# Optimization experiments

Measured on AMD Instinct MI355X. Metric: run time of the kernel, lower is better.

Reference implementation:

```python
import jax, jax.numpy as jnp
import numpy as np

DIM = 1024
N_HEADS = 16
HEAD_DIM = DIM // N_HEADS
FREQS = [31.0, 37.0, 41.0, 43.0, 47.0]
TWO_PI = 2.0 * float(np.pi)


def setup_inputs() -> dict:
    key = jax.random.key(0)
    ks = jax.random.split(key, 16)
    B, L = 2, 1024
    s = 0.02
    inp = {
        'x': jax.random.normal(ks[0], (B, L, DIM), dtype=jnp.float32),
        'Wq': jax.random.normal(ks[1], (DIM, DIM), dtype=jnp.float32) * s,
        'bq': jnp.zeros((DIM,), dtype=jnp.float32),
        'Wk': jax.random.normal(ks[2], (DIM, DIM), dtype=jnp.float32) * s,
        'bk': jnp.zeros((DIM,), dtype=jnp.float32),
        'Wv': jax.random.normal(ks[3], (DIM, DIM), dtype=jnp.float32) * s,
        'bv': jnp.zeros((DIM,), dtype=jnp.float32),
        'Wo': jax.random.normal(ks[4], (DIM, DIM), dtype=jnp.float32) * s,
        'bo': jnp.zeros((DIM,), dtype=jnp.float32),
        'alpha': jax.random.normal(ks[5], (N_HEADS, len(FREQS)), dtype=jnp.float32) * 0.1,
        'phi': jax.random.uniform(ks[6], (N_HEADS, len(FREQS)), dtype=jnp.float32) * TWO_PI,
        'temperature': jnp.ones((1,), dtype=jnp.float32),
        'gamma': jnp.ones((DIM,), dtype=jnp.float32),
        'beta': jnp.zeros((DIM,), dtype=jnp.float32),
    }
    return inp


def reference(x, Wq, bq, Wk, bk, Wv, bv, Wo, bo, alpha, phi, temperature, gamma, beta):
    B, L, D = x.shape
    H, hd = N_HEADS, HEAD_DIM
    # projections (torch Linear: y = x @ W.T + b), split heads -> (B,H,L,hd)
    q = (x @ Wq.T + bq).reshape(B, L, H, hd).transpose(0, 2, 1, 3)
    k = (x @ Wk.T + bk).reshape(B, L, H, hd).transpose(0, 2, 1, 3)
    v = (x @ Wv.T + bv).reshape(B, L, H, hd).transpose(0, 2, 1, 3)
    # similarity (B,H,L,L)
    sim = jnp.einsum('bhid,bhjd->bhij', q, k) / jnp.sqrt(jnp.asarray(hd, x.dtype))
    temp = jnp.abs(temperature)[0] + 0.1
    sim = sim / temp
    # multi-frequency holographic scores: sum_f alpha_f * sin(2*pi*sim/p_f + phi_f)
    scores = jnp.zeros_like(sim)
    for fi, freq in enumerate(FREQS):
        a = alpha[:, fi][None, :, None, None]
        p = phi[:, fi][None, :, None, None]
        scores = scores + a * jnp.sin(TWO_PI * sim / freq + p)
    # sigmoid-sum normalization (not softmax)
    w = jax.nn.sigmoid(scores)
    w = w / (jnp.sum(w, axis=-1, keepdims=True) + 1e-10)
    out = jnp.einsum('bhij,bhjd->bhid', w, v)
    out = out.transpose(0, 2, 1, 3).reshape(B, L, D)
    out = out @ Wo.T + bo
    # LayerNorm (eps=1e-5, biased variance)
    mu = jnp.mean(out, axis=-1, keepdims=True)
    var = jnp.mean(jnp.square(out - mu), axis=-1, keepdims=True)
    return (out - mu) / jnp.sqrt(var + 1e-5) * gamma + beta
```

## Files before the change

kernel.cpp:

```cpp
#include <hip/hip_runtime.h>
#include <hip/hip_bf16.h>

typedef short bf16x8 __attribute__((ext_vector_type(8)));
typedef float f32x4 __attribute__((ext_vector_type(4)));

#define MFMA16(a, b, c) __builtin_amdgcn_mfma_f32_16x16x32_bf16(a, b, c, 0, 0, 0)

static constexpr int SEQ = 1024;
static constexpr int DIM = 1024;
static constexpr int NH = 16;
static constexpr int HD = 64;

#if __has_builtin(__builtin_amdgcn_rcpf)
#define FAST_RCP(x) __builtin_amdgcn_rcpf(x)
#else
#define FAST_RCP(x) (1.0f / (x))
#endif

#if __has_builtin(__builtin_amdgcn_exp2f)
#define EXP2F(x) __builtin_amdgcn_exp2f(x)
#else
#define EXP2F(x) exp2f(x)
#endif

__device__ __forceinline__ int swz(int r) { return r ^ (r >> 3); }

__device__ __forceinline__ void gload16(const __hip_bfloat16* g, __hip_bfloat16* l)
{
    typedef const __attribute__((address_space(1))) unsigned GU;
    typedef __attribute__((address_space(3))) unsigned LU;
    __builtin_amdgcn_global_load_lds((GU*)g, (LU*)l, 16, 0, 0);
}

__global__ __launch_bounds__(256) void cvt_all(
    const float* __restrict__ x,  const float* __restrict__ wq,
    const float* __restrict__ wk, const float* __restrict__ wv,
    const float* __restrict__ wo,
    __hip_bfloat16* __restrict__ xb,  __hip_bfloat16* __restrict__ wqb,
    __hip_bfloat16* __restrict__ wkb, __hip_bfloat16* __restrict__ wvb,
    __hip_bfloat16* __restrict__ wob)
{
    const int reg = blockIdx.y;
    const float* src; __hip_bfloat16* dst; int n;
    if      (reg == 0) { src = x;  dst = xb;  n = 2 * SEQ * DIM; }
    else if (reg == 1) { src = wq; dst = wqb; n = DIM * DIM; }
    else if (reg == 2) { src = wk; dst = wkb; n = DIM * DIM; }
    else if (reg == 3) { src = wv; dst = wvb; n = DIM * DIM; }
    else               { src = wo; dst = wob; n = DIM * DIM; }
    const int i = (blockIdx.x * 256 + threadIdx.x) * 4;
    if (i < n) {
        float4 v = *(const float4*)(src + i);
        __hip_bfloat16 t[4];
        t[0] = __float2bfloat16(v.x); t[1] = __float2bfloat16(v.y);
        t[2] = __float2bfloat16(v.z); t[3] = __float2bfloat16(v.w);
        *(ushort4*)(dst + i) = *(ushort4*)t;
    }
}

__global__ __launch_bounds__(256) void gemm_qkv(
    const __hip_bfloat16* __restrict__ A,
    const __hip_bfloat16* __restrict__ W0, const __hip_bfloat16* __restrict__ W1,
    const __hip_bfloat16* __restrict__ W2,
    const float* __restrict__ b0, const float* __restrict__ b1,
    const float* __restrict__ b2,
    __hip_bfloat16* __restrict__ Y0, __hip_bfloat16* __restrict__ Y1,
    __hip_bfloat16* __restrict__ Y2,
    int M, int N, int K)
{
    __shared__ __align__(16) __hip_bfloat16 As[64 * 32];
    __shared__ __align__(16) __hip_bfloat16 Ws[128 * 32];

    const int z = blockIdx.z;
    const __hip_bfloat16* W = (z == 0) ? W0 : ((z == 1) ? W1 : W2);
    const float* bias = (z == 0) ? b0 : ((z == 1) ? b1 : b2);
    __hip_bfloat16* Y = (z == 0) ? Y0 : ((z == 1) ? Y1 : Y2);

    const int tid = threadIdx.x;
    const int wv = tid >> 6, lane = tid & 63;
    const int col16 = lane & 15, quad = lane >> 4;
    const int m0 = blockIdx.x * 64, n0 = blockIdx.y * 128;

    const __hip_bfloat16* ga = A + (size_t)(m0 + (tid >> 2)) * K + (tid & 3) * 8;
    const __hip_bfloat16* gb = W + (size_t)(n0 + (tid >> 2)) * K + (tid & 3) * 8;
    __hip_bfloat16* lA = As + wv * 512;
    __hip_bfloat16* lB = Ws + wv * 512;

    const int wr = wv >> 1, wc = wv & 1;
    const __hip_bfloat16* ar = As + (wr * 32 + col16) * 32 + quad * 8;
    const __hip_bfloat16* br = Ws + (wc * 64 + col16) * 32 + quad * 8;

    f32x4 acc[8] = {};

    for (int k0 = 0; k0 < K; k0 += 32) {
        gload16(ga + k0,                  lA);
        gload16(gb + k0,                  lB);
        gload16(gb + k0 + (size_t)64 * K, lB + 2048);
        __syncthreads();
        bf16x8 af[2], bfm[4];
#pragma unroll
        for (int mt = 0; mt < 2; ++mt) af[mt] = *(const bf16x8*)(ar + mt * 16 * 32);
#pragma unroll
        for (int nt = 0; nt < 4; ++nt) bfm[nt] = *(const bf16x8*)(br + nt * 16 * 32);
#pragma unroll
        for (int mt = 0; mt < 2; ++mt)
#pragma unroll
            for (int nt = 0; nt < 4; ++nt)
                acc[mt * 4 + nt] = MFMA16(af[mt], bfm[nt], acc[mt * 4 + nt]);
        __syncthreads();
    }

#pragma unroll
    for (int nt = 0; nt < 4; ++nt) {
        const int n = n0 + wc * 64 + nt * 16 + col16;
        const float bv = bias[n];
#pragma unroll
        for (int mt = 0; mt < 2; ++mt) {
#pragma unroll
            for (int r = 0; r < 4; ++r) {
                const int m = m0 + wr * 32 + mt * 16 + quad * 4 + r;
                Y[(size_t)m * N + n] = __float2bfloat16(acc[mt * 4 + nt][r] + bv);
            }
        }
    }
}

__global__ __launch_bounds__(256) void gemm_osplit(
    const __hip_bfloat16* __restrict__ A,
    const __hip_bfloat16* __restrict__ W,
    const float* __restrict__ bias,
    float* __restrict__ Y0, float* __restrict__ Y1,
    int M, int N, int K)
{
    __shared__ __align__(16) __hip_bfloat16 As[64 * 32];
    __shared__ __align__(16) __hip_bfloat16 Ws[128 * 32];

    const int z = blockIdx.z;
    float* Y = (z == 0) ? Y0 : Y1;
    const int kb = z * 512;

    const int tid = threadIdx.x;
    const int wv = tid >> 6, lane = tid & 63;
    const int col16 = lane & 15, quad = lane >> 4;
    const int m0 = blockIdx.x * 64, n0 = blockIdx.y * 128;

    const __hip_bfloat16* ga = A + (size_t)(m0 + (tid >> 2)) * K + (tid & 3) * 8 + kb;
    const __hip_bfloat16* gb = W + (size_t)(n0 + (tid >> 2)) * K + (tid & 3) * 8 + kb;
    __hip_bfloat16* lA = As + wv * 512;
    __hip_bfloat16* lB = Ws + wv * 512;

    const int wr = wv >> 1, wc = wv & 1;
    const __hip_bfloat16* ar = As + (wr * 32 + col16) * 32 + quad * 8;
    const __hip_bfloat16* br = Ws + (wc * 64 + col16) * 32 + quad * 8;

    f32x4 acc[8] = {};

    for (int k0 = 0; k0 < 512; k0 += 32) {
        gload16(ga + k0,                  lA);
        gload16(gb + k0,                  lB);
        gload16(gb + k0 + (size_t)64 * K, lB + 2048);
        __syncthreads();
        bf16x8 af[2], bfm[4];
#pragma unroll
        for (int mt = 0; mt < 2; ++mt) af[mt] = *(const bf16x8*)(ar + mt * 16 * 32);
#pragma unroll
        for (int nt = 0; nt < 4; ++nt) bfm[nt] = *(const bf16x8*)(br + nt * 16 * 32);
#pragma unroll
        for (int mt = 0; mt < 2; ++mt)
#pragma unroll
            for (int nt = 0; nt < 4; ++nt)
                acc[mt * 4 + nt] = MFMA16(af[mt], bfm[nt], acc[mt * 4 + nt]);
        __syncthreads();
    }

#pragma unroll
    for (int nt = 0; nt < 4; ++nt) {
        const int n = n0 + wc * 64 + nt * 16 + col16;
        const float bv = (z == 0) ? bias[n] : 0.0f;
#pragma unroll
        for (int mt = 0; mt < 2; ++mt) {
#pragma unroll
            for (int r = 0; r < 4; ++r) {
                const int m = m0 + wr * 32 + mt * 16 + quad * 4 + r;
                Y[(size_t)m * N + n] = acc[mt * 4 + nt][r] + bv;
            }
        }
    }
}

__global__ __launch_bounds__(256) void attn_kernel(
    const __hip_bfloat16* __restrict__ Q,
    const __hip_bfloat16* __restrict__ K,
    const __hip_bfloat16* __restrict__ V,
    const float* __restrict__ alpha, const float* __restrict__ phi,
    const float* __restrict__ temperature,
    __hip_bfloat16* __restrict__ AO)
{
    __shared__ __align__(16) char smem[18432 + 5120];
    __hip_bfloat16* VtBase = (__hip_bfloat16*)smem;
    __hip_bfloat16* PlBase = (__hip_bfloat16*)(smem + 18432);
    float* Ocomb = (float*)smem;
    float* Dl    = (float*)(smem + 2 * 16 * 68 * 4);

    const int tid = threadIdx.x;
    const int wv = tid >> 6, lane = tid & 63;
    const int col16 = lane & 15, quad = lane >> 4;
    const int g = wv & 1, half = wv >> 1;

    const int bh = blockIdx.y, b = bh >> 4, h = bh & 15;
    const int i0 = blockIdx.x * 32 + g * 16;
    const size_t base = ((size_t)b * SEQ) * DIM + (size_t)h * HD;

    const float tempv = fabsf(temperature[0]) + 0.1f;
    const float simscale = 1.0f / (8.0f * tempv);
    const float freqs[5] = {31.0f, 37.0f, 41.0f, 43.0f, 47.0f};

    float p[8] = {0.f, 0.f, 0.f, 0.f, 0.f, 0.f, 0.f, 0.f};
#pragma unroll
    for (int f = 0; f < 5; ++f) {
        const float a  = alpha[h * 5 + f] * 1.44269504089f;
        const float ph = phi[h * 5 + f];
        const float sp = __sinf(ph), cp = __cosf(ph);
        const float c  = 6.28318530718f * simscale / freqs[f];
        const float c2 = c * c, c3 = c2 * c, c4 = c2 * c2;
        const float c5 = c4 * c, c6 = c4 * c2, c7 = c4 * c3;
        p[0] += a * sp;
        p[1] += a * cp * c;
        p[2] -= a * sp * c2 * 0.5f;
        p[3] -= a * cp * c3 * (1.0f / 6.0f);
        p[4] += a * sp * c4 * (1.0f / 24.0f);
        p[5] += a * cp * c5 * (1.0f / 120.0f);
        p[6] -= a * sp * c6 * (1.0f / 720.0f);
        p[7] -= a * cp * c7 * (1.0f / 5040.0f);
    }

    const __hip_bfloat16* qrow = Q + base + (size_t)(i0 + col16) * DIM + quad * 8;
    const bf16x8 qa0 = *(const bf16x8*)(qrow);
    const bf16x8 qa1 = *(const bf16x8*)(qrow + 32);

    const __hip_bfloat16* kbase = K + base + (size_t)col16 * DIM + quad * 8;

    const int tl = tid & 127;
    const int sc0 = (tl & 7) * 8;
    const int sx  = tl & 7;
    const int jj0 = (tl >> 3) * 2;
    __hip_bfloat16* VtH = VtBase + half * 64 * 72;
    __hip_bfloat16* rowp[8];
#pragma unroll
    for (int e = 0; e < 8; ++e) rowp[e] = VtH + (sc0 + (e ^ sx)) * 72;

    const __hip_bfloat16* vrd[4];
#pragma unroll
    for (int t = 0; t < 4; ++t)
        vrd[t] = VtH + swz(t * 16 + col16) * 72 + quad * 8;

    __hip_bfloat16* PlW = PlBase + wv * 16 * 40;
    const __hip_bfloat16* plr = PlW + swz(col16) * 40 + quad * 8;
    __hip_bfloat16* plw[4];
#pragma unroll
    for (int r = 0; r < 4; ++r) plw[r] = PlW + swz(quad * 4 + r) * 40;

    f32x4 o[4] = {};
    float denom[4] = {0.f, 0.f, 0.f, 0.f};

    bf16x8 vr[2][2];
    bf16x8 kf[4][2];

    {
        const int j0 = half * 512;
#pragma unroll
        for (int s = 0; s < 2; ++s) {
            const __hip_bfloat16* vp = V + base + (size_t)(j0 + jj0 + 32 * s) * DIM + sc0;
            vr[s][0] = *(const bf16x8*)(vp);
            vr[s][1] = *(const bf16x8*)(vp + DIM);
        }
#pragma unroll
        for (int u = 0; u < 4; ++u) {
            const __hip_bfloat16* kp = kbase + (size_t)(j0 + u * 16) * DIM;
            kf[u][0] = *(const bf16x8*)(kp);
            kf[u][1] = *(const bf16x8*)(kp + 32);
        }
    }

    for (int it = 0; it < 8; ++it) {
        __syncthreads();
#pragma unroll
        for (int s = 0; s < 2; ++s) {
#pragma unroll
            for (int e = 0; e < 8; ++e) {
                unsigned pk = ((unsigned)(unsigned short)vr[s][0][e]) |
                              (((unsigned)(unsigned short)vr[s][1][e]) << 16);
                *(unsigned*)(rowp[e] + jj0 + 32 * s) = pk;
            }
        }
        __syncthreads();

        const int j1 = half * 512 + (it + 1) * 64;
        if (it < 7) {
#pragma unroll
            for (int s = 0; s < 2; ++s) {
                const __hip_bfloat16* vp = V + base + (size_t)(j1 + jj0 + 32 * s) * DIM + sc0;
                vr[s][0] = *(const bf16x8*)(vp);
                vr[s][1] = *(const bf16x8*)(vp + DIM);
            }
        }

        f32x4 sa4[4];
#pragma unroll
        for (int u = 0; u < 4; ++u) {
            f32x4 z = {};
            z = MFMA16(qa0, kf[u][0], z);
            z = MFMA16(qa1, kf[u][1], z);
            sa4[u] = z;
        }

        if (it < 7) {
#pragma unroll
            for (int u = 0; u < 4; ++u) {
                const __hip_bfloat16* kp = kbase + (size_t)(j1 + u * 16) * DIM;
                kf[u][0] = *(const bf16x8*)(kp);
                kf[u][1] = *(const bf16x8*)(kp + 32);
            }
        }

#pragma unroll
        for (int sub = 0; sub < 2; ++sub) {
#pragma unroll
            for (int s2 = 0; s2 < 2; ++s2) {
                const int u = sub * 2 + s2;
#pragma unroll
                for (int r = 0; r < 4; ++r) {
                    const float sv = sa4[u][r];
                    float sc = fmaf(sv, p[7], p[6]);
                    sc = fmaf(sv, sc, p[5]);
                    sc = fmaf(sv, sc, p[4]);
                    sc = fmaf(sv, sc, p[3]);
                    sc = fmaf(sv, sc, p[2]);
                    sc = fmaf(sv, sc, p[1]);
                    sc = fmaf(sv, sc, p[0]);
                    const float w = FAST_RCP(1.0f + EXP2F(-sc));
                    denom[r] += w;
                    plw[r][s2 * 16 + col16] = __float2bfloat16(w);
                }
            }
            bf16x8 pa = *(const bf16x8*)plr;
#pragma unroll
            for (int t = 0; t < 4; ++t) {
                bf16x8 vb = *(const bf16x8*)(vrd[t] + 32 * sub);
                o[t] = MFMA16(pa, vb, o[t]);
            }
        }
    }

#pragma unroll
    for (int r = 0; r < 4; ++r) {
        float d = denom[r];
        d += __shfl_xor(d, 1);
        d += __shfl_xor(d, 2);
        d += __shfl_xor(d, 4);
        d += __shfl_xor(d, 8);
        denom[r] = d;
    }

    __syncthreads();
    if (half == 1) {
#pragma unroll
        for (int t = 0; t < 4; ++t)
#pragma unroll
            for (int r = 0; r < 4; ++r)
                Ocomb[(g * 16 + quad * 4 + r) * 68 + t * 16 + col16] = o[t][r];
        if (col16 == 0) {
#pragma unroll
            for (int r = 0; r < 4; ++r) Dl[g * 16 + quad * 4 + r] = denom[r];
        }
    }
    __syncthreads();
    if (half == 0) {
#pragma unroll
        for (int r = 0; r < 4; ++r)
            denom[r] = denom[r] + Dl[g * 16 + quad * 4 + r] + 1e-10f;
#pragma unroll
        for (int t = 0; t < 4; ++t) {
#pragma unroll
            for (int r = 0; r < 4; ++r) {
                const float val =
                    (o[t][r] + Ocomb[(g * 16 + quad * 4 + r) * 68 + t * 16 + col16]) / denom[r];
                const size_t row = (size_t)b * SEQ + i0 + quad * 4 + r;
                AO[row * DIM + h * HD + t * 16 + col16] = __float2bfloat16(val);
            }
        }
    }
}

__global__ __launch_bounds__(256) void ln_kernel(
    const float* __restrict__ Yp0,
    const float* __restrict__ Yp1,
    const float* __restrict__ gamma,
    const float* __restrict__ beta,
    float* __restrict__ out)
{
    const int row = blockIdx.x;
    const float* y0 = Yp0 + (size_t)row * DIM;
    const float* y1 = Yp1 + (size_t)row * DIM;

    float v[4];
    float s = 0.f, s2 = 0.f;
#pragma unroll
    for (int e = 0; e < 4; ++e) {
        const int idx = threadIdx.x + e * 256;
        v[e] = y0[idx] + y1[idx];
        s += v[e];
        s2 += v[e] * v[e];
    }
#pragma unroll
    for (int off = 1; off < 64; off <<= 1) {
        s  += __shfl_xor(s, off);
        s2 += __shfl_xor(s2, off);
    }
    __shared__ float ps[4], ps2[4];
    const int wave = threadIdx.x >> 6;
    if ((threadIdx.x & 63) == 0) { ps[wave] = s; ps2[wave] = s2; }
    __syncthreads();
    s  = ps[0] + ps[1] + ps[2] + ps[3];
    s2 = ps2[0] + ps2[1] + ps2[2] + ps2[3];

    const float mu   = s * (1.0f / DIM);
    const float var  = s2 * (1.0f / DIM) - mu * mu;
    const float rstd = rsqrtf(var + 1e-5f);

#pragma unroll
    for (int e = 0; e < 4; ++e) {
        const int idx = threadIdx.x + e * 256;
        out[(size_t)row * DIM + idx] =
            (v[e] - mu) * rstd * gamma[idx] + beta[idx];
    }
}

extern "C" void kernel_launch(void* const* d_in, const int* in_sizes, int n_in,
                              void* d_out, int out_size, void* d_ws, size_t ws_size,
                              hipStream_t stream)
{
    const float* x     = (const float*)d_in[0];
    const float* Wq    = (const float*)d_in[1];
    const float* bq    = (const float*)d_in[2];
    const float* Wk    = (const float*)d_in[3];
    const float* bk    = (const float*)d_in[4];
    const float* Wv    = (const float*)d_in[5];
    const float* bv    = (const float*)d_in[6];
    const float* Wo    = (const float*)d_in[7];
    const float* bo    = (const float*)d_in[8];
    const float* alpha = (const float*)d_in[9];
    const float* phi   = (const float*)d_in[10];
    const float* temp  = (const float*)d_in[11];
    const float* gamma = (const float*)d_in[12];
    const float* beta  = (const float*)d_in[13];

    float* out = (float*)d_out;

    const int B = 2;
    const int M = B * SEQ;

    char* wsb = (char*)d_ws;
    __hip_bfloat16* xb  = (__hip_bfloat16*)(wsb + 0);
    __hip_bfloat16* Wqb = (__hip_bfloat16*)(wsb + (4u  << 20));
    __hip_bfloat16* Wkb = (__hip_bfloat16*)(wsb + (6u  << 20));
    __hip_bfloat16* Wvb = (__hip_bfloat16*)(wsb + (8u  << 20));
    __hip_bfloat16* Wob = (__hip_bfloat16*)(wsb + (10u << 20));
    __hip_bfloat16* Qb  = (__hip_bfloat16*)(wsb + (12u << 20));
    __hip_bfloat16* Kb  = (__hip_bfloat16*)(wsb + (16u << 20));
    __hip_bfloat16* Vb  = (__hip_bfloat16*)(wsb + (20u << 20));
    __hip_bfloat16* AO  = (__hip_bfloat16*)(wsb + (24u << 20));
    float*          Yp0 = (float*)(wsb + 0);
    float*          Yp1 = (float*)(wsb + (12u << 20));

    hipLaunchKernelGGL(cvt_all, dim3(2048, 5), dim3(256), 0, stream,
                       x, Wq, Wk, Wv, Wo, xb, Wqb, Wkb, Wvb, Wob);

    hipLaunchKernelGGL(gemm_qkv, dim3(M / 64, DIM / 128, 3), dim3(256), 0, stream,
                       xb, Wqb, Wkb, Wvb, bq, bk, bv, Qb, Kb, Vb, M, DIM, DIM);

    hipLaunchKernelGGL(attn_kernel, dim3(SEQ / 32, B * NH), dim3(256), 0, stream,
                       Qb, Kb, Vb, alpha, phi, temp, AO);

    hipLaunchKernelGGL(gemm_osplit, dim3(M / 64, DIM / 128, 2), dim3(256), 0, stream,
                       AO, Wob, bo, Yp0, Yp1, M, DIM, DIM);

    hipLaunchKernelGGL(ln_kernel, dim3(M), dim3(256), 0, stream,
                       Yp0, Yp1, gamma, beta, out);
}
```

Baseline: 177.7 us.

## Split attention key range across two blocks and add combine kernel

Adds a split-K style partition of the key dimension in the attention kernel via blockIdx.z, so each block covers half the keys and writes unnormalized fp32 partial outputs and denominators to workspace. A new combine kernel sums the partials, normalizes and writes bf16 AO. The intent is to double the number of attention blocks (from 1024 to 2048) for better occupancy and load balance on the CUs. The cost is an extra kernel launch and extra fp32 partial traffic, and the split path only runs when the workspace is at least 36 MB.

```diff
diff --git a/kernel.cpp b/kernel.cpp
--- a/kernel.cpp
+++ b/kernel.cpp
@@ -193,7 +193,9 @@
     const __hip_bfloat16* __restrict__ V,
     const float* __restrict__ alpha, const float* __restrict__ phi,
     const float* __restrict__ temperature,
-    __hip_bfloat16* __restrict__ AO)
+    float* __restrict__ Op0, float* __restrict__ Op1,
+    float* __restrict__ Dp0, float* __restrict__ Dp1,
+    __hip_bfloat16* __restrict__ AO, int nz)
 {
     __shared__ __align__(16) char smem[18432 + 5120];
     __hip_bfloat16* VtBase = (__hip_bfloat16*)smem;
@@ -209,6 +211,11 @@
     const int bh = blockIdx.y, b = bh >> 4, h = bh & 15;
     const int i0 = blockIdx.x * 32 + g * 16;
     const size_t base = ((size_t)b * SEQ) * DIM + (size_t)h * HD;
+
+    const int z = blockIdx.z;
+    const int jb = z * (SEQ / nz);
+    const int hrange = SEQ / nz / 2;
+    const int niter = hrange >> 6;
 
     const float tempv = fabsf(temperature[0]) + 0.1f;
     const float simscale = 1.0f / (8.0f * tempv);
@@ -266,7 +273,7 @@
     bf16x8 kf[4][2];
 
     {
-        const int j0 = half * 512;
+        const int j0 = jb + half * hrange;
 #pragma unroll
         for (int s = 0; s < 2; ++s) {
             const __hip_bfloat16* vp = V + base + (size_t)(j0 + jj0 + 32 * s) * DIM + sc0;
@@ -281,7 +288,7 @@
         }
     }
 
-    for (int it = 0; it < 8; ++it) {
+    for (int it = 0; it < niter; ++it) {
         __syncthreads();
 #pragma unroll
         for (int s = 0; s < 2; ++s) {
@@ -294,8 +301,8 @@
         }
         __syncthreads();
 
-        const int j1 = half * 512 + (it + 1) * 64;
-        if (it < 7) {
+        const int j1 = jb + half * hrange + (it + 1) * 64;
+        if (it + 1 < niter) {
 #pragma unroll
             for (int s = 0; s < 2; ++s) {
                 const __hip_bfloat16* vp = V + base + (size_t)(j1 + jj0 + 32 * s) * DIM + sc0;
@@ -307,13 +314,13 @@
         f32x4 sa4[4];
 #pragma unroll
         for (int u = 0; u < 4; ++u) {
-            f32x4 z = {};
-            z = MFMA16(qa0, kf[u][0], z);
-            z = MFMA16(qa1, kf[u][1], z);
-            sa4[u] = z;
-        }
-
-        if (it < 7) {
+            f32x4 zz = {};
+            zz = MFMA16(qa0, kf[u][0], zz);
+            zz = MFMA16(qa1, kf[u][1], zz);
+            sa4[u] = zz;
+        }
+
+        if (it + 1 < niter) {
 #pragma unroll
             for (int u = 0; u < 4; ++u) {
                 const __hip_bfloat16* kp = kbase + (size_t)(j1 + u * 16) * DIM;
@@ -375,20 +382,68 @@
     }
     __syncthreads();
     if (half == 0) {
-#pragma unroll
-        for (int r = 0; r < 4; ++r)
-            denom[r] = denom[r] + Dl[g * 16 + quad * 4 + r] + 1e-10f;
-#pragma unroll
-        for (int t = 0; t < 4; ++t) {
-#pragma unroll
-            for (int r = 0; r < 4; ++r) {
-                const float val =
-                    (o[t][r] + Ocomb[(g * 16 + quad * 4 + r) * 68 + t * 16 + col16]) / denom[r];
-                const size_t row = (size_t)b * SEQ + i0 + quad * 4 + r;
-                AO[row * DIM + h * HD + t * 16 + col16] = __float2bfloat16(val);
-            }
-        }
-    }
+        if (nz == 1) {
+#pragma unroll
+            for (int r = 0; r < 4; ++r)
+                denom[r] = denom[r] + Dl[g * 16 + quad * 4 + r] + 1e-10f;
+#pragma unroll
+            for (int t = 0; t < 4; ++t) {
+#pragma unroll
+                for (int r = 0; r < 4; ++r) {
+                    const float val =
+                        (o[t][r] + Ocomb[(g * 16 + quad * 4 + r) * 68 + t * 16 + col16]) / denom[r];
+                    const size_t row = (size_t)b * SEQ + i0 + quad * 4 + r;
+                    AO[row * DIM + h * HD + t * 16 + col16] = __float2bfloat16(val);
+                }
+            }
+        } else {
+            float* Op = (z == 0) ? Op0 : Op1;
+            float* Dp = (z == 0) ? Dp0 : Dp1;
+#pragma unroll
+            for (int r = 0; r < 4; ++r)
+                denom[r] = denom[r] + Dl[g * 16 + quad * 4 + r];
+            if (col16 == 0) {
+#pragma unroll
+                for (int r = 0; r < 4; ++r)
+                    Dp[(size_t)bh * SEQ + i0 + quad * 4 + r] = denom[r];
+            }
+#pragma unroll
+            for (int t = 0; t < 4; ++t) {
+#pragma unroll
+                for (int r = 0; r < 4; ++r) {
+                    const size_t prow = (size_t)bh * SEQ + i0 + quad * 4 + r;
+                    Op[prow * 64 + t * 16 + col16] =
+                        o[t][r] + Ocomb[(g * 16 + quad * 4 + r) * 68 + t * 16 + col16];
+                }
+            }
+        }
+    }
+}
+
+__global__ __launch_bounds__(256) void attn_combine(
+    const float* __restrict__ O0, const float* __restrict__ O1,
+    const float* __restrict__ D0, const float* __restrict__ D1,
+    __hip_bfloat16* __restrict__ AO)
+{
+    const int row = blockIdx.x;
+    const int b = row >> 10, i = row & 1023;
+    const int t = threadIdx.x;
+    const int h = t >> 4, dq = (t & 15) * 4;
+    const int bh = b * 16 + h;
+    const size_t prow = (size_t)bh * SEQ + i;
+    const size_t obase = prow * 64 + dq;
+
+    const float4 a0 = *(const float4*)(O0 + obase);
+    const float4 a1 = *(const float4*)(O1 + obase);
+    const float dn = D0[prow] + D1[prow] + 1e-10f;
+    const float rdn = 1.0f / dn;
+
+    __hip_bfloat16 tv[4];
+    tv[0] = __float2bfloat16((a0.x + a1.x) * rdn);
+    tv[1] = __float2bfloat16((a0.y + a1.y) * rdn);
+    tv[2] = __float2bfloat16((a0.z + a1.z) * rdn);
+    tv[3] = __float2bfloat16((a0.w + a1.w) * rdn);
+    *(ushort4*)(AO + (size_t)row * DIM + h * HD + dq) = *(ushort4*)tv;
 }
 
 __global__ __launch_bounds__(256) void ln_kernel(
@@ -471,6 +526,12 @@
     __hip_bfloat16* AO  = (__hip_bfloat16*)(wsb + (24u << 20));
     float*          Yp0 = (float*)(wsb + 0);
     float*          Yp1 = (float*)(wsb + (12u << 20));
+    float*          Op0 = (float*)(wsb + 0);
+    float*          Dp0 = (float*)(wsb + (8u << 20));
+    float*          Dp1 = (float*)(wsb + (8u << 20) + (1u << 18));
+    float*          Op1 = (float*)(wsb + (28u << 20));
+
+    const bool wide = ws_size >= (36u << 20);
 
     hipLaunchKernelGGL(cvt_all, dim3(2048, 5), dim3(256), 0, stream,
                        x, Wq, Wk, Wv, Wo, xb, Wqb, Wkb, Wvb, Wob);
@@ -478,8 +539,15 @@
     hipLaunchKernelGGL(gemm_qkv, dim3(M / 64, DIM / 128, 3), dim3(256), 0, stream,
                        xb, Wqb, Wkb, Wvb, bq, bk, bv, Qb, Kb, Vb, M, DIM, DIM);
 
-    hipLaunchKernelGGL(attn_kernel, dim3(SEQ / 32, B * NH), dim3(256), 0, stream,
-                       Qb, Kb, Vb, alpha, phi, temp, AO);
+    if (wide) {
+        hipLaunchKernelGGL(attn_kernel, dim3(SEQ / 32, B * NH, 2), dim3(256), 0, stream,
+                           Qb, Kb, Vb, alpha, phi, temp, Op0, Op1, Dp0, Dp1, AO, 2);
+        hipLaunchKernelGGL(attn_combine, dim3(M), dim3(256), 0, stream,
+                           Op0, Op1, Dp0, Dp1, AO);
+    } else {
+        hipLaunchKernelGGL(attn_kernel, dim3(SEQ / 32, B * NH, 1), dim3(256), 0, stream,
+                           Qb, Kb, Vb, alpha, phi, temp, Op0, Op1, Dp0, Dp1, AO, 1);
+    }
 
     hipLaunchKernelGGL(gemm_osplit, dim3(M / 64, DIM / 128, 2), dim3(256), 0, stream,
                        AO, Wob, bo, Yp0, Yp1, M, DIM, DIM);
```

After: 183.3 us. 1.03x slower.
